# Optimization experiments

Measured on AMD Instinct MI355X. Metric: run time of the kernel, lower is better.

## Reference

```python
import jax, jax.numpy as jnp
import numpy as np

EPS = 1e-5
NUM_HEADS = 16
NUM_KV_HEADS = 4
NUM_EXPERTS = 8
TOP_K = 2


def _layernorm(x, w, b):
    mu = jnp.mean(x, axis=-1, keepdims=True)
    var = jnp.mean((x - mu) ** 2, axis=-1, keepdims=True)
    return (x - mu) * jax.lax.rsqrt(var + EPS) * w + b


def setup_inputs() -> dict:
    key = jax.random.key(0)
    ks = jax.random.split(key, 8)
    S, B, H = 1024, 4, 1024
    F = 2048
    hd = H // NUM_HEADS
    qkv_out = (NUM_HEADS + 2 * NUM_KV_HEADS) * hd  # 1536
    w_scale = 0.02
    return {
        "hidden_states": jax.random.normal(ks[0], (S, B, H), jnp.float32),
        "ln1_weight": jnp.ones((H,), jnp.float32),
        "ln1_bias": jnp.zeros((H,), jnp.float32),
        "ln2_weight": jnp.ones((H,), jnp.float32),
        "ln2_bias": jnp.zeros((H,), jnp.float32),
        "qkv_weight": jax.random.normal(ks[1], (qkv_out, H), jnp.float32) * w_scale,
        "proj_weight": jax.random.normal(ks[2], (H, H), jnp.float32) * w_scale,
        "router_weight": jax.random.normal(ks[3], (NUM_EXPERTS, H), jnp.float32) * w_scale,
        "moe_w1": jax.random.normal(ks[4], (NUM_EXPERTS, H, F), jnp.float32) * w_scale,
        "moe_w2": jax.random.normal(ks[5], (NUM_EXPERTS, F, H), jnp.float32) * w_scale,
    }


def reference(hidden_states, ln1_weight, ln1_bias, ln2_weight, ln2_bias,
              qkv_weight, proj_weight, router_weight, moe_w1, moe_w2):
    S, B, H = hidden_states.shape
    hd = H // NUM_HEADS
    rep = NUM_HEADS // NUM_KV_HEADS
    scale = 1.0 / hd ** 0.5

    # LN1 -> fused QKV projection
    ln1_out = _layernorm(hidden_states, ln1_weight, ln1_bias)
    qkv = jnp.einsum('sbh,oh->sbo', ln1_out, qkv_weight)
    q = qkv[..., :NUM_HEADS * hd].reshape(S, B, NUM_HEADS, hd)
    k = qkv[..., NUM_HEADS * hd:(NUM_HEADS + NUM_KV_HEADS) * hd].reshape(S, B, NUM_KV_HEADS, hd)
    v = qkv[..., (NUM_HEADS + NUM_KV_HEADS) * hd:].reshape(S, B, NUM_KV_HEADS, hd)

    # GQA: repeat KV heads to match query heads
    k = jnp.repeat(k, rep, axis=2)
    v = jnp.repeat(v, rep, axis=2)

    # causal scaled dot-product attention
    scores = jnp.einsum('sbhd,tbhd->bhst', q, k) * scale  # [B,h,S,S]
    causal = jnp.tril(jnp.ones((S, S), bool))
    scores = jnp.where(causal, scores, jnp.finfo(scores.dtype).min)
    probs = jax.nn.softmax(scores, axis=-1)
    attn = jnp.einsum('bhst,tbhd->sbhd', probs, v).reshape(S, B, H)

    proj_out = jnp.einsum('sbh,oh->sbo', attn, proj_weight)
    hidden_after_attn = hidden_states + proj_out

    # LN2 -> MoE
    ln2_out = _layernorm(hidden_after_attn, ln2_weight, ln2_bias)
    x = ln2_out.reshape(-1, H)  # [T,H]

    logits = jnp.einsum('th,eh->te', x, router_weight)
    gate = jax.nn.softmax(logits, axis=-1)
    top_probs, top_idx = jax.lax.top_k(gate, TOP_K)  # [T,K]

    # dense all-expert FFN (reference for grouped expert GEMMs)
    h_mid = jax.nn.gelu(jnp.einsum('th,ehf->etf', x, moe_w1))  # [E,T,F]
    expert_out = jnp.einsum('etf,efh->eth', h_mid, moe_w2)     # [E,T,H]

    # combine: weight[e,t] = sum_k top_probs[t,k] * (top_idx[t,k]==e)
    e_ids = jnp.arange(NUM_EXPERTS)[:, None, None]
    weights = jnp.sum(jnp.where(top_idx[None] == e_ids, top_probs[None], 0.0), axis=-1)  # [E,T]
    moe_out = jnp.einsum('eth,et->th', expert_out, weights).reshape(S, B, H)

    return hidden_after_attn + moe_out
```

## Files before the change

kernel.cpp:

```cpp
#include <hip/hip_runtime.h>
#include <stdint.h>

typedef unsigned short u16;
typedef float f32x4 __attribute__((ext_vector_type(4)));
typedef __bf16 bf16x8 __attribute__((ext_vector_type(8)));
typedef u16 u16x8 __attribute__((ext_vector_type(8)));

#define NHEADS 16
#define NKV 4
#define HD 64
#define HDIM 1024
#define FDIM 2048
#define SLEN 1024
#define BATCH 4
#define TTOK 4096
#define NEXP 8
#define QKVO 1536
#define K2 2048
#define NREP 32

__device__ __forceinline__ u16 f2bf(float f) {
  union { float f; uint32_t u; } c; c.f = f;
  uint32_t u = c.u;
  return (u16)((u + 0x7FFFu + ((u >> 16) & 1u)) >> 16);
}
__device__ __forceinline__ float bf2f(u16 h) {
  union { uint32_t u; float f; } c; c.u = ((uint32_t)h) << 16; return c.f;
}
__device__ __forceinline__ void split2(float v, u16& h, u16& l) {
  h = f2bf(v);
  l = f2bf(v - bf2f(h));
}

__device__ __forceinline__ f32x4 mfma16(bf16x8 a, bf16x8 b, f32x4 c) {
  return __builtin_amdgcn_mfma_f32_16x16x32_bf16(a, b, c, 0, 0, 0);
}

__device__ __forceinline__ bf16x8 lds_frag(const u16* base) {
  u16x8 v = *(const u16x8*)base;
  return __builtin_bit_cast(bf16x8, v);
}

__device__ __forceinline__ void gload_lds16(const void* g, void* l) {
  __builtin_amdgcn_global_load_lds((const __attribute__((address_space(1))) void*)g,
                                   (__attribute__((address_space(3))) void*)l, 16, 0, 0);
}

__global__ __launch_bounds__(256)
void cvt_w2_kernel(const float* __restrict__ in, u16* __restrict__ out, int n4) {
  int i = blockIdx.x * blockDim.x + threadIdx.x;
  if (i >= n4) return;
  float4 v = ((const float4*)in)[i];
  int row = i >> 8;
  int c = (i & 255) * 4;
  ushort4 h, l;
  split2(v.x, h.x, l.x); split2(v.y, h.y, l.y);
  split2(v.z, h.z, l.z); split2(v.w, h.w, l.w);
  u16* orow = out + (size_t)row * K2 + c;
  *(ushort4*)(orow) = h;
  *(ushort4*)(orow + 1024) = l;
}

__global__ __launch_bounds__(256)
void transpose_cvt_kernel(const float* __restrict__ in, u16* __restrict__ out, int R, int C) {
  __shared__ float tile[32][33];
  size_t eoff = (size_t)blockIdx.z * (size_t)R * (size_t)C;
  in += eoff; out += eoff;
  int c0 = blockIdx.x * 32, r0 = blockIdx.y * 32;
  int tx = threadIdx.x, ty = threadIdx.y;
#pragma unroll
  for (int i = 0; i < 4; i++)
    tile[ty + i * 8][tx] = in[(size_t)(r0 + ty + i * 8) * C + c0 + tx];
  __syncthreads();
#pragma unroll
  for (int i = 0; i < 4; i++)
    out[(size_t)(c0 + ty + i * 8) * R + r0 + tx] = f2bf(tile[tx][ty + i * 8]);
}

__global__ __launch_bounds__(256)
void ln_kernel(const float* __restrict__ x, const float* __restrict__ w,
               const float* __restrict__ bias, u16* __restrict__ o2,
               u16* __restrict__ obf, float* __restrict__ of32) {
  int t = blockIdx.x, tid = threadIdx.x;
  int wid = tid >> 6, lane = tid & 63;
  float4 v = ((const float4*)(x + (size_t)t * HDIM))[tid];
  float s = v.x + v.y + v.z + v.w;
  float q = v.x * v.x + v.y * v.y + v.z * v.z + v.w * v.w;
#pragma unroll
  for (int mm = 32; mm >= 1; mm >>= 1) {
    s += __shfl_xor(s, mm);
    q += __shfl_xor(q, mm);
  }
  __shared__ float ss[4], qq[4];
  if (lane == 0) { ss[wid] = s; qq[wid] = q; }
  __syncthreads();
  s = ss[0] + ss[1] + ss[2] + ss[3];
  q = qq[0] + qq[1] + qq[2] + qq[3];
  float mu = s * (1.0f / HDIM);
  float var = q * (1.0f / HDIM) - mu * mu;
  float inv = rsqrtf(var + 1e-5f);
  float4 wv = ((const float4*)w)[tid];
  float4 bv = ((const float4*)bias)[tid];
  float y0 = (v.x - mu) * inv * wv.x + bv.x;
  float y1 = (v.y - mu) * inv * wv.y + bv.y;
  float y2 = (v.z - mu) * inv * wv.z + bv.z;
  float y3 = (v.w - mu) * inv * wv.w + bv.w;
  ushort4 h, l;
  split2(y0, h.x, l.x); split2(y1, h.y, l.y);
  split2(y2, h.z, l.z); split2(y3, h.w, l.w);
  if (o2) {
    u16* orow = o2 + (size_t)t * K2 + tid * 4;
    *(ushort4*)(orow) = h;
    *(ushort4*)(orow + 1024) = l;
  }
  if (obf) ((ushort4*)(obf + (size_t)t * HDIM))[tid] = h;
  if (of32) {
    float4 yo; yo.x = y0; yo.y = y1; yo.z = y2; yo.w = y3;
    ((float4*)(of32 + (size_t)t * HDIM))[tid] = yo;
  }
}

template<int MODE>
__global__ __launch_bounds__(256)
void gemm_bt(const u16* __restrict__ A0, const u16* __restrict__ B0,
             int kstride, int nk, int M,
             const float* __restrict__ resid, float* __restrict__ outf,
             u16* __restrict__ o0, u16* __restrict__ o1, u16* __restrict__ o2,
             u16* __restrict__ o3, u16* __restrict__ o4, u16* __restrict__ o5,
             const int* __restrict__ offs, const int* __restrict__ rowsIdx,
             const float* __restrict__ wts) {
  int tid = threadIdx.x;
  int wid = tid >> 6, lane = tid & 63;
  int l15 = lane & 15, l4 = lane >> 4;
  int slot = tid & 7;
  int bn = blockIdx.x, bm = blockIdx.y, e = blockIdx.z;

  int Me = M, rowBase = 0;
  const u16* A = A0;
  const u16* B = B0;
  if constexpr (MODE == 2 || MODE == 3) {
    int oa = offs[e], ob = offs[e + 1];
    Me = ob - oa; rowBase = oa;
    B = B0 + (size_t)e * (size_t)(MODE == 2 ? FDIM : HDIM) * (size_t)kstride;
    if constexpr (MODE == 3) A = A0 + (size_t)oa * (size_t)kstride;
  }
  if (bm * 128 >= Me) return;

  __shared__ u16 lsA[2][128 * 64];
  __shared__ u16 lsB[2][128 * 64];

  const u16* aPtr[4];
  const u16* bPtr[4];
#pragma unroll
  for (int i = 0; i < 4; i++) {
    int r = i * 32 + (tid >> 3);
    int sl = slot ^ (r & 7);
    int rg = bm * 128 + r;
    if constexpr (MODE == 2) {
      int rc = rg < Me ? rg : (Me - 1);
      rg = rowsIdx[rowBase + rc];
    } else if constexpr (MODE == 3) {
      rg = rg < Me ? rg : (Me - 1);
    }
    aPtr[i] = A + (size_t)rg * kstride + sl * 8;
    bPtr[i] = B + (size_t)(bn * 128 + r) * kstride + sl * 8;
  }

  int wm = (wid >> 1) * 64, wn = (wid & 1) * 64;
  f32x4 zero4 = {0.f, 0.f, 0.f, 0.f};
  f32x4 acc[4][4];
#pragma unroll
  for (int mi = 0; mi < 4; mi++)
#pragma unroll
    for (int ni = 0; ni < 4; ni++) acc[mi][ni] = zero4;

  int aoff[4][2], boff[4][2];
#pragma unroll
  for (int mi = 0; mi < 4; mi++) {
    int row = wm + mi * 16 + l15;
#pragma unroll
    for (int kk = 0; kk < 2; kk++) {
      int cs = kk * 4 + l4;
      aoff[mi][kk] = row * 64 + ((cs ^ (row & 7)) << 3);
    }
  }
#pragma unroll
  for (int ni = 0; ni < 4; ni++) {
    int row = wn + ni * 16 + l15;
#pragma unroll
    for (int kk = 0; kk < 2; kk++) {
      int cs = kk * 4 + l4;
      boff[ni][kk] = row * 64 + ((cs ^ (row & 7)) << 3);
    }
  }

  auto ksched = [&](int s, int& ak, int& bk, bool& stA, bool& stB) {
    if constexpr (MODE <= 1) {
      int kl = s / 3, sub = s - kl * 3;
      ak = (sub == 1 ? 1024 : 0) + kl * 64;
      bk = (sub == 2 ? 1024 : 0) + kl * 64;
      stA = (sub != 2);
      stB = (sub != 1);
    } else {
      ak = s << 6; bk = ak; stA = true; stB = true;
    }
  };

  {
    int ak, bk; bool stA, stB;
    ksched(0, ak, bk, stA, stB);
#pragma unroll
    for (int i = 0; i < 4; i++) {
      int d = (i * 256 + wid * 64) * 8;
      gload_lds16(aPtr[i] + ak, &lsA[0][d]);
      gload_lds16(bPtr[i] + bk, &lsB[0][d]);
    }
  }
  __syncthreads();

  int aBuf = 0, bBuf = 0;
  for (int s = 0; s < nk; ++s) {
    bool flipB = false;
    if (s + 1 < nk) {
      int ak, bk; bool stA, stB;
      ksched(s + 1, ak, bk, stA, stB);
      flipB = stB;
#pragma unroll
      for (int i = 0; i < 4; i++) {
        int d = (i * 256 + wid * 64) * 8;
        if (stA) gload_lds16(aPtr[i] + ak, &lsA[aBuf ^ 1][d]);
        if (stB) gload_lds16(bPtr[i] + bk, &lsB[bBuf ^ 1][d]);
      }
    }
#pragma unroll
    for (int kk = 0; kk < 2; kk++) {
      bf16x8 af[4], bfr[4];
#pragma unroll
      for (int mi = 0; mi < 4; mi++) af[mi] = lds_frag(&lsA[aBuf][aoff[mi][kk]]);
#pragma unroll
      for (int ni = 0; ni < 4; ni++) bfr[ni] = lds_frag(&lsB[bBuf][boff[ni][kk]]);
#pragma unroll
      for (int mi = 0; mi < 4; mi++)
#pragma unroll
        for (int ni = 0; ni < 4; ni++)
          acc[mi][ni] = mfma16(af[mi], bfr[ni], acc[mi][ni]);
    }
    __syncthreads();
    aBuf ^= 1;
    if (flipB) bBuf ^= 1;
  }

#pragma unroll
  for (int mi = 0; mi < 4; mi++) {
#pragma unroll
    for (int r = 0; r < 4; r++) {
      int m = bm * 128 + wm + mi * 16 + l4 * 4 + r;
      if (m >= Me) continue;
#pragma unroll
      for (int ni = 0; ni < 4; ni++) {
        int n = bn * 128 + wn + ni * 16 + l15;
        float v = acc[mi][ni][r];
        if constexpr (MODE == 0) {
          u16 hh, ll; split2(v, hh, ll);
          int sq = m >> 2, bb = m & 3;
          int d = n & 63;
          if (n < 1024) {
            int hd = n >> 6;
            size_t o = ((size_t)(bb * NHEADS + hd) * SLEN + sq) * HD + d;
            o0[o] = hh; o1[o] = ll;
          } else if (n < 1280) {
            int hd = (n - 1024) >> 6;
            size_t o = ((size_t)(bb * NKV + hd) * SLEN + sq) * HD + d;
            o2[o] = hh; o3[o] = ll;
          } else {
            int hd = (n - 1280) >> 6;
            size_t o = ((size_t)(bb * NKV + hd) * SLEN + sq) * HD + d;
            o4[o] = hh; o5[o] = ll;
          }
        } else if constexpr (MODE == 1) {
          size_t iidx = (size_t)m * HDIM + n;
          outf[iidx] = v + resid[iidx];
        } else if constexpr (MODE == 2) {
          float g = 0.5f * v * (1.0f + tanhf(0.7978845608f * (v + 0.044715f * v * v * v)));
          o0[(size_t)(rowBase + m) * FDIM + n] = f2bf(g);
        } else {
          outf[(size_t)(rowBase + m) * HDIM + n] = v * wts[rowBase + m];
        }
      }
    }
  }
}

__global__ __launch_bounds__(256)
void attn_kernel(const u16* __restrict__ Qh_, const u16* __restrict__ Ql_,
                 const u16* __restrict__ Kh_, const u16* __restrict__ Kl_,
                 const u16* __restrict__ Vh_, const u16* __restrict__ Vl_,
                 u16* __restrict__ A2) {
  int bh = blockIdx.x;
  int qt = blockIdx.y;
  int b = bh >> 4, h = bh & 15, kh = h >> 2;
  int tid = threadIdx.x, wid = tid >> 6, lane = tid & 63;
  int l15 = lane & 15, l4 = lane >> 4;
  int slot = tid & 7;

  size_t qoff = ((size_t)(b * NHEADS + h) * SLEN) * HD;
  size_t koff = ((size_t)(b * NKV + kh) * SLEN) * HD;
  const u16* Qh = Qh_ + qoff;
  const u16* Ql = Ql_ + qoff;
  const u16* Kh = Kh_ + koff;
  const u16* Kl = Kl_ + koff;
  const u16* Vh = Vh_ + koff;
  const u16* Vl = Vl_ + koff;

  __shared__ u16 KtH[2][4096], KtL[2][4096];
  __shared__ u16 VtH[4096], VtL[4096];
  __shared__ u16 PtH[4][1024], PtL[4][1024];

  int qrow = qt * 64 + wid * 16 + l15;
  bf16x8 qfh[2], qfl[2];
#pragma unroll
  for (int kk = 0; kk < 2; kk++) {
    u16x8 vh = *(const u16x8*)(Qh + (size_t)qrow * HD + kk * 32 + l4 * 8);
    u16x8 vl = *(const u16x8*)(Ql + (size_t)qrow * HD + kk * 32 + l4 * 8);
    qfh[kk] = __builtin_bit_cast(bf16x8, vh);
    qfl[kk] = __builtin_bit_cast(bf16x8, vl);
  }

  int kr0 = tid >> 3;
  int kr1 = 32 + (tid >> 3);
  int sl0 = slot ^ (kr0 & 7);
  int sl1 = slot ^ (kr1 & 7);
  int kdst0 = (0 * 256 + wid * 64) * 8;
  int kdst1 = (1 * 256 + wid * 64) * 8;

#define STAGE_K(kt_, bf_)                                                     \
  {                                                                           \
    size_t s0 = (size_t)((kt_)*64 + kr0) * HD + sl0 * 8;                      \
    size_t s1 = (size_t)((kt_)*64 + kr1) * HD + sl1 * 8;                      \
    gload_lds16(Kh + s0, &KtH[bf_][kdst0]);                                   \
    gload_lds16(Kl + s0, &KtL[bf_][kdst0]);                                   \
    gload_lds16(Kh + s1, &KtH[bf_][kdst1]);                                   \
    gload_lds16(Kl + s1, &KtL[bf_][kdst1]);                                   \
  }

#define LOAD_V(kt_, vh_, vl_)                                                 \
  {                                                                           \
    _Pragma("unroll") for (int i = 0; i < 2; i++) {                           \
      int kv = i * 32 + (tid >> 3);                                           \
      (vh_)[i] = *(const uint4*)(Vh + (size_t)((kt_)*64 + kv) * HD + slot * 8);\
      (vl_)[i] = *(const uint4*)(Vl + (size_t)((kt_)*64 + kv) * HD + slot * 8);\
    }                                                                         \
  }

#define SCATTER_V(vh_, vl_)                                                   \
  {                                                                           \
    _Pragma("unroll") for (int i = 0; i < 2; i++) {                           \
      int kv = i * 32 + (tid >> 3);                                           \
      const u16* ph = (const u16*)&(vh_)[i];                                  \
      const u16* pl = (const u16*)&(vl_)[i];                                  \
      _Pragma("unroll") for (int j = 0; j < 8; j++) {                         \
        int d = slot * 8 + j;                                                 \
        int g = ((kv >> 3) ^ (d & 7) ^ (d >> 3)) & 7;                         \
        int addr = d * 64 + (g << 3) + (kv & 7);                              \
        VtH[addr] = ph[j];                                                    \
        VtL[addr] = pl[j];                                                    \
      }                                                                       \
    }                                                                         \
  }

  uint4 vH[2], vL[2];
  STAGE_K(0, 0);
  LOAD_V(0, vH, vL);
  SCATTER_V(vH, vL);
  __syncthreads();

  f32x4 zero4 = {0.f, 0.f, 0.f, 0.f};
  f32x4 oacc[4];
#pragma unroll
  for (int nf = 0; nf < 4; nf++) oacc[nf] = zero4;
  float mrun[4], lrun[4];
#pragma unroll
  for (int r = 0; r < 4; r++) { mrun[r] = -1e30f; lrun[r] = 0.f; }

  int buf = 0;
  for (int kt = 0; kt <= qt; ++kt) {
    int kv0 = kt * 64;
    if (kt < qt) {
      STAGE_K(kt + 1, buf ^ 1);
      LOAD_V(kt + 1, vH, vL);
    }

    f32x4 sacc[4];
#pragma unroll
    for (int nf = 0; nf < 4; nf++) sacc[nf] = zero4;
#pragma unroll
    for (int kk = 0; kk < 2; kk++) {
#pragma unroll
      for (int nf = 0; nf < 4; nf++) {
        int krow = nf * 16 + l15;
        int ka = krow * 64 + (((kk * 4 + l4) ^ (krow & 7)) << 3);
        bf16x8 kfh = lds_frag(&KtH[buf][ka]);
        bf16x8 kfl = lds_frag(&KtL[buf][ka]);
        sacc[nf] = mfma16(qfh[kk], kfh, sacc[nf]);
        sacc[nf] = mfma16(qfh[kk], kfl, sacc[nf]);
        sacc[nf] = mfma16(qfl[kk], kfh, sacc[nf]);
      }
    }

    bool diag = (kt == qt);
    float tm[4];
#pragma unroll
    for (int r = 0; r < 4; r++) tm[r] = -1e30f;
#pragma unroll
    for (int nf = 0; nf < 4; nf++) {
#pragma unroll
      for (int r = 0; r < 4; r++) {
        float s = sacc[nf][r] * 0.125f;
        if (diag) {
          int qg = qt * 64 + wid * 16 + l4 * 4 + r;
          int kg = kv0 + nf * 16 + l15;
          if (kg > qg) s = -1e30f;
        }
        sacc[nf][r] = s;
        tm[r] = fmaxf(tm[r], s);
      }
    }
#pragma unroll
    for (int mm = 1; mm < 16; mm <<= 1) {
#pragma unroll
      for (int r = 0; r < 4; r++) tm[r] = fmaxf(tm[r], __shfl_xor(tm[r], mm));
    }
    float ts[4];
#pragma unroll
    for (int r = 0; r < 4; r++) {
      float mn = fmaxf(mrun[r], tm[r]);
      float al = __expf(mrun[r] - mn);
      mrun[r] = mn;
      lrun[r] *= al;
#pragma unroll
      for (int nf = 0; nf < 4; nf++) oacc[nf][r] *= al;
      ts[r] = 0.f;
    }
#pragma unroll
    for (int nf = 0; nf < 4; nf++) {
#pragma unroll
      for (int r = 0; r < 4; r++) {
        float p = __expf(sacc[nf][r] - mrun[r]);
        sacc[nf][r] = p;
        ts[r] += p;
      }
    }
#pragma unroll
    for (int mm = 1; mm < 16; mm <<= 1) {
#pragma unroll
      for (int r = 0; r < 4; r++) ts[r] += __shfl_xor(ts[r], mm);
    }
#pragma unroll
    for (int r = 0; r < 4; r++) lrun[r] += ts[r];

#pragma unroll
    for (int nf = 0; nf < 4; nf++) {
#pragma unroll
      for (int r = 0; r < 4; r++) {
        int qrl = l4 * 4 + r;
        int kv = nf * 16 + l15;
        int g = ((kv >> 3) ^ (qrl & 7) ^ (qrl >> 3)) & 7;
        int addr = qrl * 64 + (g << 3) + (kv & 7);
        u16 hh, ll;
        split2(sacc[nf][r], hh, ll);
        PtH[wid][addr] = hh;
        PtL[wid][addr] = ll;
      }
    }
#pragma unroll
    for (int s2 = 0; s2 < 2; s2++) {
      int cs = s2 * 4 + l4;
      int pa = l15 * 64 + ((((cs ^ (l15 & 7) ^ (l15 >> 3))) & 7) << 3);
      bf16x8 pfh = lds_frag(&PtH[wid][pa]);
      bf16x8 pfl = lds_frag(&PtL[wid][pa]);
#pragma unroll
      for (int nf = 0; nf < 4; nf++) {
        int d = nf * 16 + l15;
        int va = d * 64 + ((((cs ^ (d & 7) ^ (d >> 3))) & 7) << 3);
        bf16x8 vfh = lds_frag(&VtH[va]);
        bf16x8 vfl = lds_frag(&VtL[va]);
        oacc[nf] = mfma16(pfh, vfh, oacc[nf]);
        oacc[nf] = mfma16(pfh, vfl, oacc[nf]);
        oacc[nf] = mfma16(pfl, vfh, oacc[nf]);
      }
    }

    __syncthreads();
    if (kt < qt) {
      SCATTER_V(vH, vL);
    }
    __syncthreads();
    buf ^= 1;
  }

#pragma unroll
  for (int r = 0; r < 4; r++) {
    float invl = 1.0f / lrun[r];
    int qg = qt * 64 + wid * 16 + l4 * 4 + r;
    size_t tb = ((size_t)qg * BATCH + b) * K2 + h * HD;
#pragma unroll
    for (int nf = 0; nf < 4; nf++) {
      u16 hh, ll;
      split2(oacc[nf][r] * invl, hh, ll);
      size_t o = tb + nf * 16 + l15;
      A2[o] = hh;
      A2[o + 1024] = ll;
    }
  }
#undef STAGE_K
#undef LOAD_V
#undef SCATTER_V
}

__global__ __launch_bounds__(256)
void router_kernel(const float* __restrict__ x, const float* __restrict__ rw,
                   int* __restrict__ tidx, float* __restrict__ tp) {
  int t = blockIdx.x, tid = threadIdx.x;
  int wid = tid >> 6, lane = tid & 63;
  float4 xv = ((const float4*)(x + (size_t)t * HDIM))[tid];
  __shared__ float part[8][4];
  __shared__ float lg[8];
#pragma unroll
  for (int e = 0; e < 8; e++) {
    float4 wv = ((const float4*)(rw + (size_t)e * HDIM))[tid];
    float d = xv.x * wv.x + xv.y * wv.y + xv.z * wv.z + xv.w * wv.w;
#pragma unroll
    for (int mm = 32; mm >= 1; mm >>= 1) d += __shfl_xor(d, mm);
    if (lane == 0) part[e][wid] = d;
  }
  __syncthreads();
  if (tid < 8) lg[tid] = part[tid][0] + part[tid][1] + part[tid][2] + part[tid][3];
  __syncthreads();
  if (tid == 0) {
    float mx = lg[0];
#pragma unroll
    for (int e = 1; e < 8; e++) mx = fmaxf(mx, lg[e]);
    float g[8]; float se = 0.f;
#pragma unroll
    for (int e = 0; e < 8; e++) { g[e] = __expf(lg[e] - mx); se += g[e]; }
    float inv = 1.0f / se;
#pragma unroll
    for (int e = 0; e < 8; e++) g[e] *= inv;
    int i0 = 0; float v0 = g[0];
#pragma unroll
    for (int e = 1; e < 8; e++) if (g[e] > v0) { v0 = g[e]; i0 = e; }
    int i1 = -1; float v1 = -1.f;
#pragma unroll
    for (int e = 0; e < 8; e++) if (e != i0 && g[e] > v1) { v1 = g[e]; i1 = e; }
    tidx[t * 2] = i0; tidx[t * 2 + 1] = i1;
    tp[t * 2] = v0; tp[t * 2 + 1] = v1;
  }
}

__global__ __launch_bounds__(256)
void hist_offsets_kernel(const int* __restrict__ tidx, int* __restrict__ offs,
                         int* __restrict__ repBase, int* __restrict__ curRep) {
  __shared__ int hist[NEXP * NREP];
  __shared__ int eoffs[NEXP + 1];
  int tid = threadIdx.x;
  hist[tid] = 0;
  __syncthreads();
  for (int i = tid; i < TTOK; i += 256) {
    int rep = i & (NREP - 1);
    atomicAdd(&hist[tidx[2 * i] * NREP + rep], 1);
    atomicAdd(&hist[tidx[2 * i + 1] * NREP + rep], 1);
  }
  __syncthreads();
  if (tid == 0) {
    int a = 0;
    for (int e = 0; e < NEXP; e++) {
      eoffs[e] = a;
      for (int r = 0; r < NREP; r++) a += hist[e * NREP + r];
    }
    eoffs[NEXP] = a;
  }
  __syncthreads();
  if (tid < NEXP) {
    int a = eoffs[tid];
    for (int r = 0; r < NREP; r++) {
      repBase[tid * NREP + r] = a;
      a += hist[tid * NREP + r];
    }
  }
  if (tid < NEXP + 1) offs[tid] = eoffs[tid];
  curRep[tid] = 0;
}

__global__ __launch_bounds__(256)
void assign_kernel(const int* __restrict__ tidx, const float* __restrict__ tp,
                   const int* __restrict__ repBase, int* __restrict__ curRep,
                   int* __restrict__ rowsIdx, float* __restrict__ wvals,
                   int* __restrict__ inv) {
  int t = blockIdx.x * blockDim.x + threadIdx.x;
  if (t >= TTOK) return;
  int rep = t & (NREP - 1);
#pragma unroll
  for (int k = 0; k < 2; k++) {
    int e = tidx[t * 2 + k];
    int s = atomicAdd(&curRep[e * NREP + rep], 1);
    int pos = repBase[e * NREP + rep] + s;
    rowsIdx[pos] = t;
    wvals[pos] = tp[t * 2 + k];
    inv[t * 2 + k] = pos;
  }
}

__global__ __launch_bounds__(256)
void combine_kernel(float* __restrict__ out, const float* __restrict__ eo,
                    const int* __restrict__ inv) {
  int t = blockIdx.x, c = threadIdx.x;
  int r0 = inv[t * 2], r1 = inv[t * 2 + 1];
  float4* o = (float4*)(out + (size_t)t * HDIM);
  const float4* e0 = (const float4*)(eo + (size_t)r0 * HDIM);
  const float4* e1 = (const float4*)(eo + (size_t)r1 * HDIM);
  float4 v = o[c];
  float4 a = e0[c];
  float4 bb = e1[c];
  v.x += a.x + bb.x; v.y += a.y + bb.y; v.z += a.z + bb.z; v.w += a.w + bb.w;
  o[c] = v;
}

extern "C" void kernel_launch(void* const* d_in, const int* in_sizes, int n_in,
                              void* d_out, int out_size, void* d_ws, size_t ws_size,
                              hipStream_t stream) {
  (void)in_sizes; (void)n_in; (void)out_size; (void)ws_size;
  const float* hs    = (const float*)d_in[0];
  const float* ln1w  = (const float*)d_in[1];
  const float* ln1b  = (const float*)d_in[2];
  const float* ln2w  = (const float*)d_in[3];
  const float* ln2b  = (const float*)d_in[4];
  const float* wqkv  = (const float*)d_in[5];
  const float* wproj = (const float*)d_in[6];
  const float* wrout = (const float*)d_in[7];
  const float* w1    = (const float*)d_in[8];
  const float* w2    = (const float*)d_in[9];
  float* out = (float*)d_out;

  char* base = (char*)d_ws;
  size_t off = 0;
  auto alloc = [&](size_t n) { void* r = base + off; off += (n + 255) & ~(size_t)255; return r; };

  const size_t SZ_W1T   = (size_t)NEXP * FDIM * HDIM * 2;
  const size_t SZ_W2T   = (size_t)NEXP * HDIM * FDIM * 2;
  const size_t SZ_WP2   = (size_t)HDIM * K2 * 2;
  const size_t SZ_LN12  = (size_t)TTOK * K2 * 2;
  const size_t SZ_WQ2   = (size_t)QKVO * K2 * 2;
  const size_t SZ_HMID  = (size_t)TTOK * 2 * FDIM * 2;
  const size_t SZ_Q     = (size_t)BATCH * NHEADS * SLEN * HD * 2;
  const size_t SZ_KV    = (size_t)BATCH * NKV * SLEN * HD * 2;
  const size_t SZ_A2    = (size_t)TTOK * K2 * 2;
  const size_t SZ_EO    = (size_t)TTOK * 2 * HDIM * 4;

  u16* w1t     = (u16*)alloc(SZ_W1T);
  u16* w2t     = (u16*)alloc(SZ_W2T);
  u16* wproj2  = (u16*)alloc(SZ_WP2);

  size_t r1sz = SZ_LN12 + SZ_WQ2;
  if (SZ_HMID > r1sz) r1sz = SZ_HMID;
  char* r1 = (char*)alloc(r1sz);
  u16* ln1_2 = (u16*)r1;
  u16* wqkv2 = (u16*)(r1 + SZ_LN12);
  u16* hmid  = (u16*)r1;

  size_t r2sz = 2 * SZ_Q + 4 * SZ_KV + SZ_A2;
  if (SZ_EO > r2sz) r2sz = SZ_EO;
  char* r2 = (char*)alloc(r2sz);
  u16* Qbh = (u16*)r2;
  u16* Qbl = (u16*)(r2 + SZ_Q);
  u16* Kbh = (u16*)(r2 + 2 * SZ_Q);
  u16* Kbl = (u16*)(r2 + 2 * SZ_Q + SZ_KV);
  u16* Vbh = (u16*)(r2 + 2 * SZ_Q + 2 * SZ_KV);
  u16* Vbl = (u16*)(r2 + 2 * SZ_Q + 3 * SZ_KV);
  u16* attn2 = (u16*)(r2 + 2 * SZ_Q + 4 * SZ_KV);
  float* eo = (float*)r2;

  u16* ln2o    = (u16*)alloc((size_t)TTOK * HDIM * 2);
  float* ln2f  = (float*)alloc((size_t)TTOK * HDIM * 4);
  int* tidx    = (int*)alloc(TTOK * 2 * 4);
  float* tp    = (float*)alloc(TTOK * 2 * 4);
  int* rowsIdx = (int*)alloc(TTOK * 2 * 4);
  float* wvals = (float*)alloc(TTOK * 2 * 4);
  int* invm    = (int*)alloc(TTOK * 2 * 4);
  int* offs    = (int*)alloc((NEXP + 1) * 4);
  int* repBase = (int*)alloc(NEXP * NREP * 4);
  int* curRep  = (int*)alloc(NEXP * NREP * 4);

  cvt_w2_kernel<<<(QKVO * HDIM / 4 + 255) / 256, 256, 0, stream>>>(wqkv, wqkv2, QKVO * HDIM / 4);
  cvt_w2_kernel<<<(HDIM * HDIM / 4 + 255) / 256, 256, 0, stream>>>(wproj, wproj2, HDIM * HDIM / 4);
  dim3 tb(32, 8);
  transpose_cvt_kernel<<<dim3(FDIM / 32, HDIM / 32, NEXP), tb, 0, stream>>>(w1, w1t, HDIM, FDIM);
  transpose_cvt_kernel<<<dim3(HDIM / 32, FDIM / 32, NEXP), tb, 0, stream>>>(w2, w2t, FDIM, HDIM);

  ln_kernel<<<TTOK, 256, 0, stream>>>(hs, ln1w, ln1b, ln1_2, nullptr, nullptr);

  gemm_bt<0><<<dim3(QKVO / 128, TTOK / 128), 256, 0, stream>>>(
      ln1_2, wqkv2, K2, 48, TTOK, nullptr, nullptr,
      Qbh, Qbl, Kbh, Kbl, Vbh, Vbl, nullptr, nullptr, nullptr);

  attn_kernel<<<dim3(BATCH * NHEADS, SLEN / 64), 256, 0, stream>>>(
      Qbh, Qbl, Kbh, Kbl, Vbh, Vbl, attn2);

  gemm_bt<1><<<dim3(HDIM / 128, TTOK / 128), 256, 0, stream>>>(
      attn2, wproj2, K2, 48, TTOK, hs, out,
      nullptr, nullptr, nullptr, nullptr, nullptr, nullptr, nullptr, nullptr, nullptr);

  ln_kernel<<<TTOK, 256, 0, stream>>>(out, ln2w, ln2b, nullptr, ln2o, ln2f);

  router_kernel<<<TTOK, 256, 0, stream>>>(ln2f, wrout, tidx, tp);
  hist_offsets_kernel<<<1, 256, 0, stream>>>(tidx, offs, repBase, curRep);
  assign_kernel<<<TTOK / 256, 256, 0, stream>>>(tidx, tp, repBase, curRep, rowsIdx, wvals, invm);

  gemm_bt<2><<<dim3(FDIM / 128, TTOK / 128, NEXP), 256, 0, stream>>>(
      ln2o, w1t, HDIM, 16, 0, nullptr, nullptr,
      hmid, nullptr, nullptr, nullptr, nullptr, nullptr, offs, rowsIdx, nullptr);

  gemm_bt<3><<<dim3(HDIM / 128, TTOK / 128, NEXP), 256, 0, stream>>>(
      hmid, w2t, FDIM, 32, 0, nullptr, eo,
      nullptr, nullptr, nullptr, nullptr, nullptr, nullptr, offs, nullptr, wvals);

  combine_kernel<<<TTOK, 256, 0, stream>>>(out, eo, invm);
}
```

Baseline: 462.9 us.

## Add 256x256-tile 8-wave grouped GEMM kernel for MoE expert FFNs

```diff
diff --git a/kernel.cpp b/kernel.cpp
--- a/kernel.cpp
+++ b/kernel.cpp
@@ -126,25 +126,12 @@
              int kstride, int nk, int M,
              const float* __restrict__ resid, float* __restrict__ outf,
              u16* __restrict__ o0, u16* __restrict__ o1, u16* __restrict__ o2,
-             u16* __restrict__ o3, u16* __restrict__ o4, u16* __restrict__ o5,
-             const int* __restrict__ offs, const int* __restrict__ rowsIdx,
-             const float* __restrict__ wts) {
+             u16* __restrict__ o3, u16* __restrict__ o4, u16* __restrict__ o5) {
   int tid = threadIdx.x;
   int wid = tid >> 6, lane = tid & 63;
   int l15 = lane & 15, l4 = lane >> 4;
   int slot = tid & 7;
-  int bn = blockIdx.x, bm = blockIdx.y, e = blockIdx.z;
-
-  int Me = M, rowBase = 0;
-  const u16* A = A0;
-  const u16* B = B0;
-  if constexpr (MODE == 2 || MODE == 3) {
-    int oa = offs[e], ob = offs[e + 1];
-    Me = ob - oa; rowBase = oa;
-    B = B0 + (size_t)e * (size_t)(MODE == 2 ? FDIM : HDIM) * (size_t)kstride;
-    if constexpr (MODE == 3) A = A0 + (size_t)oa * (size_t)kstride;
-  }
-  if (bm * 128 >= Me) return;
+  int bn = blockIdx.x, bm = blockIdx.y;
 
   __shared__ u16 lsA[2][128 * 64];
   __shared__ u16 lsB[2][128 * 64];
@@ -155,15 +142,8 @@
   for (int i = 0; i < 4; i++) {
     int r = i * 32 + (tid >> 3);
     int sl = slot ^ (r & 7);
-    int rg = bm * 128 + r;
-    if constexpr (MODE == 2) {
-      int rc = rg < Me ? rg : (Me - 1);
-      rg = rowsIdx[rowBase + rc];
-    } else if constexpr (MODE == 3) {
-      rg = rg < Me ? rg : (Me - 1);
-    }
-    aPtr[i] = A + (size_t)rg * kstride + sl * 8;
-    bPtr[i] = B + (size_t)(bn * 128 + r) * kstride + sl * 8;
+    aPtr[i] = A0 + (size_t)(bm * 128 + r) * kstride + sl * 8;
+    bPtr[i] = B0 + (size_t)(bn * 128 + r) * kstride + sl * 8;
   }
 
   int wm = (wid >> 1) * 64, wn = (wid & 1) * 64;
@@ -195,15 +175,11 @@
   }
 
   auto ksched = [&](int s, int& ak, int& bk, bool& stA, bool& stB) {
-    if constexpr (MODE <= 1) {
-      int kl = s / 3, sub = s - kl * 3;
-      ak = (sub == 1 ? 1024 : 0) + kl * 64;
-      bk = (sub == 2 ? 1024 : 0) + kl * 64;
-      stA = (sub != 2);
-      stB = (sub != 1);
-    } else {
-      ak = s << 6; bk = ak; stA = true; stB = true;
-    }
+    int kl = s / 3, sub = s - kl * 3;
+    ak = (sub == 1 ? 1024 : 0) + kl * 64;
+    bk = (sub == 2 ? 1024 : 0) + kl * 64;
+    stA = (sub != 2);
+    stB = (sub != 1);
   };
 
   {
@@ -255,7 +231,6 @@
 #pragma unroll
     for (int r = 0; r < 4; r++) {
       int m = bm * 128 + wm + mi * 16 + l4 * 4 + r;
-      if (m >= Me) continue;
 #pragma unroll
       for (int ni = 0; ni < 4; ni++) {
         int n = bn * 128 + wn + ni * 16 + l15;
@@ -277,12 +252,143 @@
             size_t o = ((size_t)(bb * NKV + hd) * SLEN + sq) * HD + d;
             o4[o] = hh; o5[o] = ll;
           }
-        } else if constexpr (MODE == 1) {
+        } else {
           size_t iidx = (size_t)m * HDIM + n;
           outf[iidx] = v + resid[iidx];
-        } else if constexpr (MODE == 2) {
-          float g = 0.5f * v * (1.0f + tanhf(0.7978845608f * (v + 0.044715f * v * v * v)));
-          o0[(size_t)(rowBase + m) * FDIM + n] = f2bf(g);
+        }
+      }
+    }
+  }
+}
+
+template<int MODE>
+__global__ __launch_bounds__(512)
+void gemm8(const u16* __restrict__ A0, const u16* __restrict__ B0,
+           int kstride, int nk,
+           float* __restrict__ outf, u16* __restrict__ o0,
+           const int* __restrict__ offs, const int* __restrict__ rowsIdx,
+           const float* __restrict__ wts) {
+  int tid = threadIdx.x;
+  int wid = tid >> 6, lane = tid & 63;
+  int l15 = lane & 15, l4 = lane >> 4;
+  int bn = blockIdx.x, bm = blockIdx.y, e = blockIdx.z;
+  constexpr int N = (MODE == 2 ? FDIM : HDIM);
+
+  int oa = offs[e], ob = offs[e + 1];
+  int Me = ob - oa, rowBase = oa;
+  const u16* A = A0;
+  const u16* B = B0 + (size_t)e * (size_t)N * (size_t)kstride;
+  if constexpr (MODE == 3) A = A0 + (size_t)oa * (size_t)kstride;
+  if (bm * 256 >= Me) return;
+
+  __shared__ u16 ls[2][2][2][256 * 32];
+
+  const u16* aSrc[2];
+  const u16* bSrc[2];
+#pragma unroll
+  for (int i = 0; i < 2; i++) {
+    int s = i * 512 + tid;
+    int r = s >> 2, sl = s & 3;
+    int logs = sl ^ ((r >> 1) & 3);
+    int rg = bm * 256 + r;
+    if constexpr (MODE == 2) {
+      int rc = rg < Me ? rg : (Me - 1);
+      rg = rowsIdx[rowBase + rc];
+    } else {
+      rg = rg < Me ? rg : (Me - 1);
+    }
+    aSrc[i] = A + (size_t)rg * kstride + logs * 8;
+    bSrc[i] = B + (size_t)(bn * 256 + r) * kstride + logs * 8;
+  }
+
+  auto stageA = [&](int t_, int h) {
+#pragma unroll
+    for (int i = 0; i < 2; i++)
+      gload_lds16(aSrc[i] + t_ * 64 + h * 32,
+                  &ls[0][t_ & 1][h][(i * 512 + wid * 64) * 8]);
+  };
+  auto stageB = [&](int t_, int h) {
+#pragma unroll
+    for (int i = 0; i < 2; i++)
+      gload_lds16(bSrc[i] + t_ * 64 + h * 32,
+                  &ls[1][t_ & 1][h][(i * 512 + wid * 64) * 8]);
+  };
+
+  int wm = wid >> 2, wn = wid & 3;
+  f32x4 zero4 = {0.f, 0.f, 0.f, 0.f};
+  f32x4 acc[8][4];
+#pragma unroll
+  for (int mi = 0; mi < 8; mi++)
+#pragma unroll
+    for (int ni = 0; ni < 4; ni++) acc[mi][ni] = zero4;
+
+  int aoff[8], boff[4];
+#pragma unroll
+  for (int mi = 0; mi < 8; mi++) {
+    int rr = wm * 128 + mi * 16 + l15;
+    aoff[mi] = rr * 32 + ((l4 ^ ((rr >> 1) & 3)) * 8);
+  }
+#pragma unroll
+  for (int ni = 0; ni < 4; ni++) {
+    int rn = wn * 64 + ni * 16 + l15;
+    boff[ni] = rn * 32 + ((l4 ^ ((rn >> 1) & 3)) * 8);
+  }
+
+  stageA(0, 0); stageB(0, 0);
+  stageA(0, 1); stageB(0, 1);
+  stageA(1, 0); stageB(1, 0);
+  asm volatile("s_waitcnt vmcnt(4)" ::: "memory");
+  __builtin_amdgcn_s_barrier();
+
+  for (int t = 0; t < nk; ++t) {
+    int buf = t & 1;
+#pragma unroll
+    for (int p = 0; p < 4; ++p) {
+      constexpr int KKTAB[4] = {0, 0, 1, 1};
+      const int kk = KKTAB[p];
+      const int g = p & 1;
+      bf16x8 af[4], bfr[4];
+#pragma unroll
+      for (int j = 0; j < 4; j++)
+        af[j] = lds_frag(&ls[0][buf][kk][aoff[g * 4 + j]]);
+#pragma unroll
+      for (int j = 0; j < 4; j++)
+        bfr[j] = lds_frag(&ls[1][buf][kk][boff[j]]);
+      if (p == 0) { if (t + 1 < nk) stageA(t + 1, 1); }
+      else if (p == 1) { if (t + 1 < nk) stageB(t + 1, 1); }
+      else if (p == 2) { if (t + 2 < nk) stageA(t + 2, 0); }
+      else { if (t + 2 < nk) stageB(t + 2, 0); }
+      __builtin_amdgcn_s_barrier();
+      __builtin_amdgcn_s_setprio(1);
+#pragma unroll
+      for (int j = 0; j < 4; j++)
+#pragma unroll
+        for (int ni = 0; ni < 4; ni++)
+          acc[g * 4 + j][ni] = mfma16(af[j], bfr[ni], acc[g * 4 + j][ni]);
+      __builtin_amdgcn_s_setprio(0);
+      if (p == 3) {
+        if (t + 1 < nk) {
+          if (t + 2 < nk) asm volatile("s_waitcnt vmcnt(4)" ::: "memory");
+          else            asm volatile("s_waitcnt vmcnt(0)" ::: "memory");
+        }
+      }
+      __builtin_amdgcn_s_barrier();
+    }
+  }
+
+#pragma unroll
+  for (int mi = 0; mi < 8; mi++) {
+#pragma unroll
+    for (int r = 0; r < 4; r++) {
+      int m = bm * 256 + wm * 128 + mi * 16 + l4 * 4 + r;
+      if (m >= Me) continue;
+#pragma unroll
+      for (int ni = 0; ni < 4; ni++) {
+        int n = bn * 256 + wn * 64 + ni * 16 + l15;
+        float v = acc[mi][ni][r];
+        if constexpr (MODE == 2) {
+          float g2 = 0.5f * v * (1.0f + tanhf(0.7978845608f * (v + 0.044715f * v * v * v)));
+          o0[(size_t)(rowBase + m) * FDIM + n] = f2bf(g2);
         } else {
           outf[(size_t)(rowBase + m) * HDIM + n] = v * wts[rowBase + m];
         }
@@ -700,14 +806,14 @@
 
   gemm_bt<0><<<dim3(QKVO / 128, TTOK / 128), 256, 0, stream>>>(
       ln1_2, wqkv2, K2, 48, TTOK, nullptr, nullptr,
-      Qbh, Qbl, Kbh, Kbl, Vbh, Vbl, nullptr, nullptr, nullptr);
+      Qbh, Qbl, Kbh, Kbl, Vbh, Vbl);
 
   attn_kernel<<<dim3(BATCH * NHEADS, SLEN / 64), 256, 0, stream>>>(
       Qbh, Qbl, Kbh, Kbl, Vbh, Vbl, attn2);
 
   gemm_bt<1><<<dim3(HDIM / 128, TTOK / 128), 256, 0, stream>>>(
       attn2, wproj2, K2, 48, TTOK, hs, out,
-      nullptr, nullptr, nullptr, nullptr, nullptr, nullptr, nullptr, nullptr, nullptr);
+      nullptr, nullptr, nullptr, nullptr, nullptr, nullptr);
 
   ln_kernel<<<TTOK, 256, 0, stream>>>(out, ln2w, ln2b, nullptr, ln2o, ln2f);
 
@@ -715,13 +821,11 @@
   hist_offsets_kernel<<<1, 256, 0, stream>>>(tidx, offs, repBase, curRep);
   assign_kernel<<<TTOK / 256, 256, 0, stream>>>(tidx, tp, repBase, curRep, rowsIdx, wvals, invm);
 
-  gemm_bt<2><<<dim3(FDIM / 128, TTOK / 128, NEXP), 256, 0, stream>>>(
-      ln2o, w1t, HDIM, 16, 0, nullptr, nullptr,
-      hmid, nullptr, nullptr, nullptr, nullptr, nullptr, offs, rowsIdx, nullptr);
-
-  gemm_bt<3><<<dim3(HDIM / 128, TTOK / 128, NEXP), 256, 0, stream>>>(
-      hmid, w2t, FDIM, 32, 0, nullptr, eo,
-      nullptr, nullptr, nullptr, nullptr, nullptr, nullptr, offs, nullptr, wvals);
+  gemm8<2><<<dim3(FDIM / 256, TTOK / 256, NEXP), 512, 0, stream>>>(
+      ln2o, w1t, HDIM, 16, nullptr, hmid, offs, rowsIdx, nullptr);
+
+  gemm8<3><<<dim3(HDIM / 256, TTOK / 256, NEXP), 512, 0, stream>>>(
+      hmid, w2t, FDIM, 32, eo, nullptr, offs, nullptr, wvals);
 
   combine_kernel<<<TTOK, 256, 0, stream>>>(out, eo, invm);
 }
```

New measurement: 472.6 us. 1.02x slower.

## Add dedicated 256x128-tile MoE W1 GEMM with shared B tile and K=32 steps

Applied to the files above, without the earlier changes.

```diff
diff --git a/kernel.cpp b/kernel.cpp
--- a/kernel.cpp
+++ b/kernel.cpp
@@ -292,6 +292,119 @@
 }
 
 __global__ __launch_bounds__(256)
+void gemm_w1(const u16* __restrict__ A0, const u16* __restrict__ B0,
+             int kstride, int nk,
+             u16* __restrict__ o0,
+             const int* __restrict__ offs, const int* __restrict__ rowsIdx) {
+  int tid = threadIdx.x;
+  int wid = tid >> 6, lane = tid & 63;
+  int l15 = lane & 15, l4 = lane >> 4;
+  int bn = blockIdx.x, bm = blockIdx.y, e = blockIdx.z;
+
+  int oa = offs[e], ob = offs[e + 1];
+  int Me = ob - oa, rowBase = oa;
+  const u16* B = B0 + (size_t)e * (size_t)FDIM * (size_t)kstride;
+  if (bm * 256 >= Me) return;
+
+  __shared__ u16 lsA[2][2][128 * 32];
+  __shared__ u16 lsB[2][128 * 32];
+
+  const u16* aSrc[2][2];
+  const u16* bSrc[2];
+#pragma unroll
+  for (int i = 0; i < 2; i++) {
+    int s = i * 256 + tid;
+    int r = s >> 2, sl = s & 3;
+    int logs = sl ^ ((r >> 1) & 3);
+#pragma unroll
+    for (int j = 0; j < 2; j++) {
+      int rg = bm * 256 + j * 128 + r;
+      int rc = rg < Me ? rg : (Me - 1);
+      rc = rowsIdx[rowBase + rc];
+      aSrc[j][i] = A0 + (size_t)rc * kstride + logs * 8;
+    }
+    bSrc[i] = B + (size_t)(bn * 128 + r) * kstride + logs * 8;
+  }
+
+  int wm = (wid >> 1) * 64, wn = (wid & 1) * 64;
+  f32x4 zero4 = {0.f, 0.f, 0.f, 0.f};
+  f32x4 acc[2][4][4];
+#pragma unroll
+  for (int j = 0; j < 2; j++)
+#pragma unroll
+    for (int mi = 0; mi < 4; mi++)
+#pragma unroll
+      for (int ni = 0; ni < 4; ni++) acc[j][mi][ni] = zero4;
+
+  int aoff[4], boff[4];
+#pragma unroll
+  for (int mi = 0; mi < 4; mi++) {
+    int row = wm + mi * 16 + l15;
+    aoff[mi] = row * 32 + ((l4 ^ ((row >> 1) & 3)) * 8);
+  }
+#pragma unroll
+  for (int ni = 0; ni < 4; ni++) {
+    int rn = wn + ni * 16 + l15;
+    boff[ni] = rn * 32 + ((l4 ^ ((rn >> 1) & 3)) * 8);
+  }
+
+  auto stage = [&](int s, int buf) {
+    int k0 = s * 32;
+#pragma unroll
+    for (int j = 0; j < 2; j++)
+#pragma unroll
+      for (int i = 0; i < 2; i++)
+        gload_lds16(aSrc[j][i] + k0, &lsA[buf][j][(i * 256 + wid * 64) * 8]);
+#pragma unroll
+    for (int i = 0; i < 2; i++)
+      gload_lds16(bSrc[i] + k0, &lsB[buf][(i * 256 + wid * 64) * 8]);
+  };
+
+  stage(0, 0);
+  __syncthreads();
+
+  int buf = 0;
+  for (int s = 0; s < nk; ++s) {
+    if (s + 1 < nk) stage(s + 1, buf ^ 1);
+    bf16x8 bfr[4];
+#pragma unroll
+    for (int ni = 0; ni < 4; ni++) bfr[ni] = lds_frag(&lsB[buf][boff[ni]]);
+#pragma unroll
+    for (int j = 0; j < 2; j++) {
+      bf16x8 af[4];
+#pragma unroll
+      for (int mi = 0; mi < 4; mi++) af[mi] = lds_frag(&lsA[buf][j][aoff[mi]]);
+#pragma unroll
+      for (int mi = 0; mi < 4; mi++)
+#pragma unroll
+        for (int ni = 0; ni < 4; ni++)
+          acc[j][mi][ni] = mfma16(af[mi], bfr[ni], acc[j][mi][ni]);
+    }
+    __syncthreads();
+    buf ^= 1;
+  }
+
+#pragma unroll
+  for (int j = 0; j < 2; j++) {
+#pragma unroll
+    for (int mi = 0; mi < 4; mi++) {
+#pragma unroll
+      for (int r = 0; r < 4; r++) {
+        int m = bm * 256 + j * 128 + wm + mi * 16 + l4 * 4 + r;
+        if (m >= Me) continue;
+#pragma unroll
+        for (int ni = 0; ni < 4; ni++) {
+          int n = bn * 128 + wn + ni * 16 + l15;
+          float v = acc[j][mi][ni][r];
+          float g = 0.5f * v * (1.0f + tanhf(0.7978845608f * (v + 0.044715f * v * v * v)));
+          o0[(size_t)(rowBase + m) * FDIM + n] = f2bf(g);
+        }
+      }
+    }
+  }
+}
+
+__global__ __launch_bounds__(256)
 void attn_kernel(const u16* __restrict__ Qh_, const u16* __restrict__ Ql_,
                  const u16* __restrict__ Kh_, const u16* __restrict__ Kl_,
                  const u16* __restrict__ Vh_, const u16* __restrict__ Vl_,
@@ -715,9 +828,8 @@
   hist_offsets_kernel<<<1, 256, 0, stream>>>(tidx, offs, repBase, curRep);
   assign_kernel<<<TTOK / 256, 256, 0, stream>>>(tidx, tp, repBase, curRep, rowsIdx, wvals, invm);
 
-  gemm_bt<2><<<dim3(FDIM / 128, TTOK / 128, NEXP), 256, 0, stream>>>(
-      ln2o, w1t, HDIM, 16, 0, nullptr, nullptr,
-      hmid, nullptr, nullptr, nullptr, nullptr, nullptr, offs, rowsIdx, nullptr);
+  gemm_w1<<<dim3(FDIM / 128, TTOK / 256, NEXP), 256, 0, stream>>>(
+      ln2o, w1t, HDIM, HDIM / 32, hmid, offs, rowsIdx);
 
   gemm_bt<3><<<dim3(HDIM / 128, TTOK / 128, NEXP), 256, 0, stream>>>(
       hmid, w2t, FDIM, 32, 0, nullptr, eo,
```

Result: slower. 515.1 us (+11.3%).
